# Kernel optimization log

Measured on AMD Instinct MI355X. Metric: run time of the kernel, lower is better.

The kernel has to match this reference:

```python
import jax, jax.numpy as jnp
import numpy as np

N_NODES = 100000


def _l2norm(v, eps=1e-12):
    return v / (jnp.linalg.norm(v) + eps)


def setup_inputs() -> dict:
    key = jax.random.key(0)
    k1, k2, k3, k4 = jax.random.split(key, 4)
    x = jax.random.normal(k1, (N_NODES, 128), dtype=jnp.float32)
    edge_index = jax.random.randint(k2, (2, 600000), 0, N_NODES, dtype=jnp.int64)
    # GCNConv weight [in, out] (xavier-ish scale), bias zeros (default init)
    W = jax.random.normal(k3, (128, 64), dtype=jnp.float32) * (1.0 / np.sqrt(128))
    bias = jnp.zeros((64,), dtype=jnp.float32)
    # learnable edge_wt initialized to ones (torch.ones_like(edge_weight))
    ew = jnp.ones((600000,), dtype=jnp.float32)
    # spectral-norm persistent power-iteration vector u (len = W.shape[0])
    u = jax.random.normal(k4, (128,), dtype=jnp.float32)
    return {"x": x, "edge_index": edge_index, "W": W, "bias": bias, "ew": ew, "u": u}


def gcn_forward(x, edge_index, W, bias, ew, u):
    N = x.shape[0]
    # --- spectral norm: one power-iteration step (u, v under stop_gradient) ---
    v = jax.lax.stop_gradient(_l2norm(W.T @ u))          # [out]
    u2 = jax.lax.stop_gradient(_l2norm(W @ v))           # [in]
    sigma = u2 @ (W @ v)
    W_sn = W / sigma
    # --- GCNConv with sigmoid edge weights, self-loops (weight 1), sym norm ---
    w = jax.nn.sigmoid(ew)                               # [E]
    row, col = edge_index[0], edge_index[1]
    deg = jax.ops.segment_sum(w, col, num_segments=N) + 1.0  # +1 from self-loop
    dis = jax.lax.rsqrt(deg)                             # deg > 0 always
    xp = x @ W_sn                                        # [N, out]
    norm_e = dis[row] * w * dis[col]                     # [E]
    msg = xp[row] * norm_e[:, None]                      # gather + scale
    agg = jax.ops.segment_sum(msg, col, num_segments=N)  # scatter-add
    out = agg + xp * (1.0 / deg)[:, None] + bias         # self-loop norm = deg^-1
    return out


def reference(x, edge_index, W, bias, ew, u):
    return gcn_forward(x, edge_index, W, bias, ew, u)
```

## Files before the change

### kernel.cpp

```cpp
#include <hip/hip_runtime.h>
#include <math.h>


#define IN_DIM 128
#define OUT_DIM 64

#define FIXSHIFT 4294967296.0
#define CNTSHIFT 40
#define DEGMASK  ((1ull << CNTSHIFT) - 1)

#define CAP    64
#define CAPLOG 6

typedef __attribute__((ext_vector_type(4))) short s16x4;
typedef __attribute__((ext_vector_type(8))) short s16x8;
typedef __attribute__((ext_vector_type(4))) float f32x4;

__device__ __forceinline__ short f2bf(float f) {
    unsigned int v = __float_as_uint(f);
    v = v + 0x7FFFu + ((v >> 16) & 1u);
    return (short)(v >> 16);
}
__device__ __forceinline__ float bfLo(unsigned int v) {
    return __uint_as_float(v << 16);
}
__device__ __forceinline__ float bfHi(unsigned int v) {
    return __uint_as_float(v & 0xFFFF0000u);
}

#define APITCH 136

__global__ __launch_bounds__(256) void fused(const float* __restrict__ x,
                                             const int* __restrict__ ei,
                                             const float* __restrict__ W,
                                             const float* __restrict__ ew,
                                             const float* __restrict__ u,
                                             unsigned long long* __restrict__ packed,
                                             int2* __restrict__ spk,
                                             unsigned short* __restrict__ xps,
                                             float* __restrict__ inv_sigma,
                                             int N, int E, int ntile, int G) {
    __shared__ __align__(16) short Wt[64 * APITCH];

    const int t = threadIdx.x;
    const int bid = blockIdx.x;

    if (bid == G - 1) {
        float* red = (float*)Wt;
        float* vsh = (float*)(Wt + 512);
        {
            const int j = t & 63;
            const int i0 = (t >> 6) * 32;
            float tv = 0.f;
            #pragma unroll 8
            for (int i = 0; i < 32; ++i) tv += W[(i0 + i) * OUT_DIM + j] * u[i0 + i];
            red[t] = tv;
        }
        __syncthreads();
        float tvj = 0.f;
        if (t < 64) tvj = red[t] + red[t + 64] + red[t + 128] + red[t + 192];
        __syncthreads();
        red[t] = (t < 64) ? tvj * tvj : 0.f;
        __syncthreads();
        for (int sr = 128; sr > 0; sr >>= 1) {
            if (t < sr) red[t] += red[t + sr];
            __syncthreads();
        }
        const float nv = sqrtf(red[0]) + 1e-12f;
        __syncthreads();
        if (t < 64) vsh[t] = tvj / nv;
        __syncthreads();
        float wv = 0.f;
        if (t < 128) {
            #pragma unroll 8
            for (int j = 0; j < OUT_DIM; ++j) wv += W[t * OUT_DIM + j] * vsh[j];
        }
        red[t] = (t < 128) ? wv * wv : 0.f;
        __syncthreads();
        for (int sr = 128; sr > 0; sr >>= 1) {
            if (t < sr) red[t] += red[t + sr];
            __syncthreads();
        }
        if (t == 0) {
            const float s2 = red[0];
            const float sn = sqrtf(s2);
            inv_sigma[0] = (sn + 1e-12f) / s2;
        }
        return;
    }

    const int pair = bid >> 1;

    if ((bid & 1) == 0) {
        const int e = pair * 256 + t;
        if (e >= E) return;
        const float w = 1.f / (1.f + expf(-ew[e]));
        const int row = ei[e];
        const int col = ei[E + e];
        const unsigned long long inc =
            (1ull << CNTSHIFT) | (unsigned long long)((double)w * FIXSHIFT);
        const unsigned long long old = atomicAdd(&packed[col], inc);
        const int slot = (int)(old >> CNTSHIFT);
        if (slot < CAP) {
            int2 pk; pk.x = row; pk.y = __float_as_int(w);
            spk[((size_t)col << CAPLOG) + slot] = pk;
        }
        return;
    }

    const int tile = pair;
    if (tile >= ntile) return;
    const int r0 = tile * 64;

    {
        #pragma unroll
        for (int p = 0; p < 2; ++p) {
            const int k  = p * 64 + (t >> 2);
            const int n0 = (t & 3) * 16;
            const float4* wsrc = (const float4*)(W + (size_t)k * OUT_DIM + n0);
            #pragma unroll
            for (int i = 0; i < 4; ++i) {
                const float4 v = wsrc[i];
                Wt[(n0 + 4 * i + 0) * APITCH + k] = f2bf(v.x);
                Wt[(n0 + 4 * i + 1) * APITCH + k] = f2bf(v.y);
                Wt[(n0 + 4 * i + 2) * APITCH + k] = f2bf(v.z);
                Wt[(n0 + 4 * i + 3) * APITCH + k] = f2bf(v.w);
            }
        }
    }
    __syncthreads();

    const int wave = t >> 6;
    const int lane = t & 63;
    const int m    = lane & 15;
    const int quad = lane >> 4;

    const int grow_a = min(r0 + wave * 16 + m, N - 1);
    const float* arow = x + (size_t)grow_a * IN_DIM + quad * 8;

    f32x4 acc[4];
    #pragma unroll
    for (int ct = 0; ct < 4; ++ct) acc[ct] = (f32x4){0.f, 0.f, 0.f, 0.f};

    const short* Bbase = &Wt[m * APITCH + quad * 8];

    #pragma unroll
    for (int kc = 0; kc < 4; ++kc) {
        const float4 f0 = *(const float4*)(arow + kc * 32);
        const float4 f1 = *(const float4*)(arow + kc * 32 + 4);
        s16x8 a;
        a[0] = f2bf(f0.x); a[1] = f2bf(f0.y); a[2] = f2bf(f0.z); a[3] = f2bf(f0.w);
        a[4] = f2bf(f1.x); a[5] = f2bf(f1.y); a[6] = f2bf(f1.z); a[7] = f2bf(f1.w);
        #pragma unroll
        for (int ct = 0; ct < 4; ++ct) {
            const s16x8 b = *(const s16x8*)(Bbase + ct * 16 * APITCH + kc * 32);
            acc[ct] = __builtin_amdgcn_mfma_f32_16x16x32_bf16(a, b, acc[ct], 0, 0, 0);
        }
    }

    #pragma unroll
    for (int r = 0; r < 4; ++r) {
        const int grow = r0 + wave * 16 + quad * 4 + r;
        if (grow < N) {
            #pragma unroll
            for (int ct = 0; ct < 4; ++ct)
                xps[(size_t)grow * OUT_DIM + ct * 16 + m] =
                    (unsigned short)f2bf(acc[ct][r]);
        }
    }
}

__global__ __launch_bounds__(256) void gather(const int2* __restrict__ spk,
                                              const unsigned long long* __restrict__ packed,
                                              const uint4* __restrict__ xps128,
                                              const float* __restrict__ bias,
                                              const float* __restrict__ inv_sigma,
                                              float* __restrict__ out,
                                              int N) {
    const int t = threadIdx.x;
    const int q  = t >> 3;
    const int el = t & 7;
    const int n = blockIdx.x * 32 + q;
    if (n >= N) return;

    const unsigned long long p = packed[n];
    const int c = min((int)(p >> CNTSHIFT), CAP);
    const float deg = (float)((double)(p & DEGMASK) * (1.0 / FIXSHIFT));
    const size_t st = (size_t)n << CAPLOG;

    const uint4 sv = xps128[(size_t)n * 8 + el];
    const float isg = inv_sigma[0];

    float a0 = 0.f, a1 = 0.f, a2 = 0.f, a3 = 0.f;
    float a4 = 0.f, a5 = 0.f, a6 = 0.f, a7 = 0.f;

    for (int j0 = 0; j0 < c; j0 += 8) {
        const int rem = c - j0;
        int2 e; e.x = 0; e.y = 0;
        if (el < rem) e = spk[st + j0 + el];

        #pragma unroll
        for (int k = 0; k < 8; k += 4) {
            if (!__any(rem > k)) break;
            #pragma unroll
            for (int kk = 0; kk < 4; ++kk) {
                const int row = __shfl(e.x, k + kk, 8);
                const float wraw = __int_as_float(__shfl(e.y, k + kk, 8));
                const unsigned long long pr = packed[row];
                const uint4 a = xps128[(size_t)row * 8 + el];
                const float degr = (float)((double)(pr & DEGMASK) * (1.0 / FIXSHIFT));
                const float w = wraw * rsqrtf(degr + 1.f);
                a0 += bfLo(a.x) * w;
                a1 += bfHi(a.x) * w;
                a2 += bfLo(a.y) * w;
                a3 += bfHi(a.y) * w;
                a4 += bfLo(a.z) * w;
                a5 += bfHi(a.z) * w;
                a6 += bfLo(a.w) * w;
                a7 += bfHi(a.w) * w;
            }
        }
    }

    const float dfull = deg + 1.f;
    const float dis_n = rsqrtf(dfull);
    const float invd  = 1.f / dfull;
    const float4 bv0 = ((const float4*)bias)[el * 2];
    const float4 bv1 = ((const float4*)bias)[el * 2 + 1];
    float4 o0, o1;
    o0.x = isg * (dis_n * a0 + bfLo(sv.x) * invd) + bv0.x;
    o0.y = isg * (dis_n * a1 + bfHi(sv.x) * invd) + bv0.y;
    o0.z = isg * (dis_n * a2 + bfLo(sv.y) * invd) + bv0.z;
    o0.w = isg * (dis_n * a3 + bfHi(sv.y) * invd) + bv0.w;
    o1.x = isg * (dis_n * a4 + bfLo(sv.z) * invd) + bv1.x;
    o1.y = isg * (dis_n * a5 + bfHi(sv.z) * invd) + bv1.y;
    o1.z = isg * (dis_n * a6 + bfLo(sv.w) * invd) + bv1.z;
    o1.w = isg * (dis_n * a7 + bfHi(sv.w) * invd) + bv1.w;
    ((float4*)out)[(size_t)n * 16 + el * 2] = o0;
    ((float4*)out)[(size_t)n * 16 + el * 2 + 1] = o1;
}

extern "C" void kernel_launch(void* const* d_in, const int* in_sizes, int n_in,
                              void* d_out, int out_size, void* d_ws, size_t ws_size,
                              hipStream_t stream) {
    const float* x    = (const float*)d_in[0];
    const int*   ei   = (const int*)d_in[1];
    const float* W    = (const float*)d_in[2];
    const float* bias = (const float*)d_in[3];
    const float* ew   = (const float*)d_in[4];
    const float* u    = (const float*)d_in[5];
    float* out = (float*)d_out;

    const int N = in_sizes[0] / IN_DIM;
    const int E = in_sizes[4];
    const int EB = (E + 255) / 256;
    const int ntile = (N + 63) / 64;

    char* ws = (char*)d_ws;
    size_t off = 0;
    unsigned long long* packed = (unsigned long long*)(ws + off); off += (size_t)N * 8;
    float* isg  = (float*)(ws + off); off += 1024;
    unsigned short* xps = (unsigned short*)(ws + off); off += (size_t)N * OUT_DIM * 2;
    int2*  spk  = (int2*) (ws + off); off += (size_t)N * CAP * 8;

    const int mx = (EB > ntile) ? EB : ntile;
    const int G = 2 * mx + 1;

    hipMemsetAsync(packed, 0, (size_t)N * 8, stream);
    fused<<<G, 256, 0, stream>>>(x, ei, W, ew, u, packed, spk, xps, isg,
                                 N, E, ntile, G);
    gather<<<(N + 31) / 32, 256, 0, stream>>>(spk, packed, (const uint4*)xps,
                                              bias, isg, out, N);
}
```

Before: 158.8 us.

## Batch edges and GEMM tiles per block, fully unroll gather inner loop

Edge-scatter blocks now handle two edges per thread and issue both loads before the atomics, so more memory traffic is in flight. GEMM blocks loop over four 64-row tiles, so the bf16 transpose of W into shared memory is paid once per four tiles instead of once per tile. Together these roughly halve the fused grid. The gather loop drops the early-exit vote and always unrolls 8 neighbour slots. For short neighbour lists this adds padded loads of row 0 with zero weight, in exchange for more independent loads in flight.

```diff
diff --git a/kernel.cpp b/kernel.cpp
--- a/kernel.cpp
+++ b/kernel.cpp
@@ -29,6 +29,7 @@
 }
 
 #define APITCH 136
+#define TPB    4
 
 __global__ __launch_bounds__(256) void fused(const float* __restrict__ x,
                                              const int* __restrict__ ei,
@@ -39,7 +40,7 @@
                                              int2* __restrict__ spk,
                                              unsigned short* __restrict__ xps,
                                              float* __restrict__ inv_sigma,
-                                             int N, int E, int ntile, int G) {
+                                             int N, int E, int ntile4, int G) {
     __shared__ __align__(16) short Wt[64 * APITCH];
 
     const int t = threadIdx.x;
@@ -92,25 +93,45 @@
     const int pair = bid >> 1;
 
     if ((bid & 1) == 0) {
-        const int e = pair * 256 + t;
-        if (e >= E) return;
-        const float w = 1.f / (1.f + expf(-ew[e]));
-        const int row = ei[e];
-        const int col = ei[E + e];
-        const unsigned long long inc =
-            (1ull << CNTSHIFT) | (unsigned long long)((double)w * FIXSHIFT);
-        const unsigned long long old = atomicAdd(&packed[col], inc);
-        const int slot = (int)(old >> CNTSHIFT);
-        if (slot < CAP) {
-            int2 pk; pk.x = row; pk.y = __float_as_int(w);
-            spk[((size_t)col << CAPLOG) + slot] = pk;
+        const int e0 = pair * 512 + t;
+        const int e1 = e0 + 256;
+        const bool v0 = e0 < E;
+        const bool v1 = e1 < E;
+        int row0 = 0, col0 = 0, row1 = 0, col1 = 0;
+        float w0 = 0.f, w1 = 0.f;
+        if (v0) {
+            row0 = ei[e0]; col0 = ei[E + e0];
+            w0 = 1.f / (1.f + expf(-ew[e0]));
+        }
+        if (v1) {
+            row1 = ei[e1]; col1 = ei[E + e1];
+            w1 = 1.f / (1.f + expf(-ew[e1]));
+        }
+        if (v0) {
+            const unsigned long long inc =
+                (1ull << CNTSHIFT) | (unsigned long long)((double)w0 * FIXSHIFT);
+            const unsigned long long old = atomicAdd(&packed[col0], inc);
+            const int slot = (int)(old >> CNTSHIFT);
+            if (slot < CAP) {
+                int2 pk; pk.x = row0; pk.y = __float_as_int(w0);
+                spk[((size_t)col0 << CAPLOG) + slot] = pk;
+            }
+        }
+        if (v1) {
+            const unsigned long long inc =
+                (1ull << CNTSHIFT) | (unsigned long long)((double)w1 * FIXSHIFT);
+            const unsigned long long old = atomicAdd(&packed[col1], inc);
+            const int slot = (int)(old >> CNTSHIFT);
+            if (slot < CAP) {
+                int2 pk; pk.x = row1; pk.y = __float_as_int(w1);
+                spk[((size_t)col1 << CAPLOG) + slot] = pk;
+            }
         }
         return;
     }
 
-    const int tile = pair;
-    if (tile >= ntile) return;
-    const int r0 = tile * 64;
+    const int tq = pair;
+    if (tq >= ntile4) return;
 
     {
         #pragma unroll
@@ -134,38 +155,43 @@
     const int lane = t & 63;
     const int m    = lane & 15;
     const int quad = lane >> 4;
-
-    const int grow_a = min(r0 + wave * 16 + m, N - 1);
-    const float* arow = x + (size_t)grow_a * IN_DIM + quad * 8;
-
-    f32x4 acc[4];
+    const short* Bbase = &Wt[m * APITCH + quad * 8];
+
     #pragma unroll
-    for (int ct = 0; ct < 4; ++ct) acc[ct] = (f32x4){0.f, 0.f, 0.f, 0.f};
-
-    const short* Bbase = &Wt[m * APITCH + quad * 8];
-
-    #pragma unroll
-    for (int kc = 0; kc < 4; ++kc) {
-        const float4 f0 = *(const float4*)(arow + kc * 32);
-        const float4 f1 = *(const float4*)(arow + kc * 32 + 4);
-        s16x8 a;
-        a[0] = f2bf(f0.x); a[1] = f2bf(f0.y); a[2] = f2bf(f0.z); a[3] = f2bf(f0.w);
-        a[4] = f2bf(f1.x); a[5] = f2bf(f1.y); a[6] = f2bf(f1.z); a[7] = f2bf(f1.w);
-        #pragma unroll
-        for (int ct = 0; ct < 4; ++ct) {
-            const s16x8 b = *(const s16x8*)(Bbase + ct * 16 * APITCH + kc * 32);
-            acc[ct] = __builtin_amdgcn_mfma_f32_16x16x32_bf16(a, b, acc[ct], 0, 0, 0);
-        }
-    }
-
-    #pragma unroll
-    for (int r = 0; r < 4; ++r) {
-        const int grow = r0 + wave * 16 + quad * 4 + r;
-        if (grow < N) {
+    for (int s = 0; s < TPB; ++s) {
+        const int r0 = tq * (TPB * 64) + s * 64;
+        if (r0 >= N) break;
+
+        const int grow_a = min(r0 + wave * 16 + m, N - 1);
+        const float* arow = x + (size_t)grow_a * IN_DIM + quad * 8;
+
+        f32x4 acc[4];
+        #pragma unroll
+        for (int ct = 0; ct < 4; ++ct) acc[ct] = (f32x4){0.f, 0.f, 0.f, 0.f};
+
+        #pragma unroll
+        for (int kc = 0; kc < 4; ++kc) {
+            const float4 f0 = *(const float4*)(arow + kc * 32);
+            const float4 f1 = *(const float4*)(arow + kc * 32 + 4);
+            s16x8 a;
+            a[0] = f2bf(f0.x); a[1] = f2bf(f0.y); a[2] = f2bf(f0.z); a[3] = f2bf(f0.w);
+            a[4] = f2bf(f1.x); a[5] = f2bf(f1.y); a[6] = f2bf(f1.z); a[7] = f2bf(f1.w);
             #pragma unroll
-            for (int ct = 0; ct < 4; ++ct)
-                xps[(size_t)grow * OUT_DIM + ct * 16 + m] =
-                    (unsigned short)f2bf(acc[ct][r]);
+            for (int ct = 0; ct < 4; ++ct) {
+                const s16x8 b = *(const s16x8*)(Bbase + ct * 16 * APITCH + kc * 32);
+                acc[ct] = __builtin_amdgcn_mfma_f32_16x16x32_bf16(a, b, acc[ct], 0, 0, 0);
+            }
+        }
+
+        #pragma unroll
+        for (int r = 0; r < 4; ++r) {
+            const int grow = r0 + wave * 16 + quad * 4 + r;
+            if (grow < N) {
+                #pragma unroll
+                for (int ct = 0; ct < 4; ++ct)
+                    xps[(size_t)grow * OUT_DIM + ct * 16 + m] =
+                        (unsigned short)f2bf(acc[ct][r]);
+            }
         }
     }
 }
@@ -200,25 +226,21 @@
         if (el < rem) e = spk[st + j0 + el];
 
         #pragma unroll
-        for (int k = 0; k < 8; k += 4) {
-            if (!__any(rem > k)) break;
-            #pragma unroll
-            for (int kk = 0; kk < 4; ++kk) {
-                const int row = __shfl(e.x, k + kk, 8);
-                const float wraw = __int_as_float(__shfl(e.y, k + kk, 8));
-                const unsigned long long pr = packed[row];
-                const uint4 a = xps128[(size_t)row * 8 + el];
-                const float degr = (float)((double)(pr & DEGMASK) * (1.0 / FIXSHIFT));
-                const float w = wraw * rsqrtf(degr + 1.f);
-                a0 += bfLo(a.x) * w;
-                a1 += bfHi(a.x) * w;
-                a2 += bfLo(a.y) * w;
-                a3 += bfHi(a.y) * w;
-                a4 += bfLo(a.z) * w;
-                a5 += bfHi(a.z) * w;
-                a6 += bfLo(a.w) * w;
-                a7 += bfHi(a.w) * w;
-            }
+        for (int k = 0; k < 8; ++k) {
+            const int row = __shfl(e.x, k, 8);
+            const float wraw = __int_as_float(__shfl(e.y, k, 8));
+            const unsigned long long pr = packed[row];
+            const uint4 a = xps128[(size_t)row * 8 + el];
+            const float degr = (float)((double)(pr & DEGMASK) * (1.0 / FIXSHIFT));
+            const float w = wraw * rsqrtf(degr + 1.f);
+            a0 += bfLo(a.x) * w;
+            a1 += bfHi(a.x) * w;
+            a2 += bfLo(a.y) * w;
+            a3 += bfHi(a.y) * w;
+            a4 += bfLo(a.z) * w;
+            a5 += bfHi(a.z) * w;
+            a6 += bfLo(a.w) * w;
+            a7 += bfHi(a.w) * w;
         }
     }
 
@@ -253,8 +275,8 @@
 
     const int N = in_sizes[0] / IN_DIM;
     const int E = in_sizes[4];
-    const int EB = (E + 255) / 256;
-    const int ntile = (N + 63) / 64;
+    const int EB2 = (E + 511) / 512;
+    const int ntile4 = (N + TPB * 64 - 1) / (TPB * 64);
 
     char* ws = (char*)d_ws;
     size_t off = 0;
@@ -263,12 +285,12 @@
     unsigned short* xps = (unsigned short*)(ws + off); off += (size_t)N * OUT_DIM * 2;
     int2*  spk  = (int2*) (ws + off); off += (size_t)N * CAP * 8;
 
-    const int mx = (EB > ntile) ? EB : ntile;
+    const int mx = (EB2 > ntile4) ? EB2 : ntile4;
     const int G = 2 * mx + 1;
 
     hipMemsetAsync(packed, 0, (size_t)N * 8, stream);
     fused<<<G, 256, 0, stream>>>(x, ei, W, ew, u, packed, spk, xps, isg,
-                                 N, E, ntile, G);
+                                 N, E, ntile4, G);
     gather<<<(N + 31) / 32, 256, 0, stream>>>(spk, packed, (const uint4*)xps,
                                               bias, isg, out, N);
 }
```

Result: slower. 169.2 us (+6.5%).
